# Performance work log

Hardware: AMD Instinct MI355X
Metric: run time of the kernel (lower is better)

## Reference

```python
import jax, jax.numpy as jnp
import numpy as np
from jax import lax

HEADS = 8
HEAD_C = 16  # attention_channels // heads = 128 // 8


def setup_inputs() -> dict:
    key = jax.random.key(0)
    ks = jax.random.split(key, 16)
    N, I, H, W = 8, 128, 36, 36
    R, C, A, O = 128, 128, 128, 128  # recurrent, common, attention, out channels
    s = lambda *sh: 0.05
    inp = {
        'x': jax.random.normal(ks[0], (N, I, H, W), jnp.float32),
        # input 1x1 conv (Accumulate of single Conv, bias init 0)
        'w_in': jax.random.normal(ks[1], (R, I), jnp.float32) * 0.05,
        'b_in': jnp.zeros((R,), jnp.float32),
        # 3x3 conv on cat([x, h]) -> common channels
        'w_conv': jax.random.normal(ks[2], (C, 2 * R, 3, 3), jnp.float32) * 0.05,
        'b_conv': jnp.zeros((C,), jnp.float32),
        # q/k/v 1x1 projections (no bias)
        'wq': jax.random.normal(ks[3], (A, C), jnp.float32) * 0.05,
        'wk': jax.random.normal(ks[4], (A, C), jnp.float32) * 0.05,
        'wv': jax.random.normal(ks[5], (A, C), jnp.float32) * 0.05,
        # gate 1x1 projections on cat([z, a]) (C + A inputs)
        'w_i': jax.random.normal(ks[6], (R, C + A), jnp.float32) * 0.05,
        'b_i': jnp.full((R,), -1.0, jnp.float32),  # init_input
        'w_f': jax.random.normal(ks[7], (R, C + A), jnp.float32) * 0.05,
        'b_f': jnp.full((R,), 1.0, jnp.float32),   # init_forget
        'w_g': jax.random.normal(ks[8], (R, C + A), jnp.float32) * 0.05,
        'b_g': jnp.zeros((R,), jnp.float32),
        'w_o': jax.random.normal(ks[9], (R, C + A), jnp.float32) * 0.05,
        'b_o': jnp.zeros((R,), jnp.float32),
        # output 1x1 conv
        'w_out': jax.random.normal(ks[10], (O, R), jnp.float32) * 0.05,
        'b_out': jnp.zeros((O,), jnp.float32),
    }
    return inp


def _conv1x1(w, x, b=None):
    y = jnp.einsum('oi,nihw->nohw', w, x)
    if b is not None:
        y = y + b[None, :, None, None]
    return y


def reference(x, w_in, b_in, w_conv, b_conv, wq, wk, wv,
              w_i, b_i, w_f, b_f, w_g, b_g, w_o, b_o, w_out, b_out):
    # first timestep: past is empty -> h = c = 0
    xt = jnp.tanh(_conv1x1(w_in, x, b_in))          # [N, R, H, W]
    h0 = jnp.zeros_like(xt)
    c0 = jnp.zeros_like(xt)
    xh = jnp.concatenate([xt, h0], axis=1)          # groups=1 -> plain concat
    z = lax.conv_general_dilated(xh, w_conv, (1, 1), 'SAME') + b_conv[None, :, None, None]
    N, C, H, W = z.shape
    HW = H * W
    q = _conv1x1(wq, z).reshape(N, HEADS, HEAD_C, HW)
    k = _conv1x1(wk, z).reshape(N, HEADS, HEAD_C, HW)
    v = _conv1x1(wv, z).reshape(N, HEADS, HEAD_C, HW)
    # spatial attention over H*W tokens per head
    w_attn = jax.nn.softmax(jnp.einsum('nhcq,nhcd->nhqd', q, k), axis=-1)  # [N,heads,HW,HW]
    a = jnp.einsum('nhcd,nhqd->nhcq', v, w_attn).reshape(N, -1, H, W)      # [N,A,H,W]
    za = jnp.concatenate([z, a], axis=1)
    i = jax.nn.sigmoid(_conv1x1(w_i, za, b_i))
    f = jax.nn.sigmoid(_conv1x1(w_f, za, b_f))
    g = jnp.tanh(_conv1x1(w_g, za, b_g))
    o = jax.nn.sigmoid(_conv1x1(w_o, za, b_o))
    c = f * c0 + i * g
    h = o * jnp.tanh(c)  # dropout p=0 -> identity
    return _conv1x1(w_out, h, b_out)
```

## Files before the change

### kernel.cpp

```cpp
#include <hip/hip_runtime.h>
#include <hip/hip_bf16.h>
#include <math.h>

typedef __hip_bfloat16 bf16;
typedef __attribute__((ext_vector_type(8))) short frag8;
typedef __attribute__((ext_vector_type(4))) float f32x4;
typedef __attribute__((ext_vector_type(16))) float f32x16;
typedef __attribute__((ext_vector_type(2))) unsigned int u32x2;
typedef __attribute__((ext_vector_type(4))) unsigned int u32x4;

#define HW  1296
#define CH  128
#define TT  1327104

__device__ __forceinline__ float b2f(bf16 v) { return __bfloat162float(v); }
__device__ __forceinline__ float bits2f(unsigned short u) {
    return __uint_as_float(((unsigned)u) << 16);
}
__device__ __forceinline__ float frcp(float x) { return __builtin_amdgcn_rcpf(x); }
__device__ __forceinline__ float fsigm(float x) { return frcp(1.0f + __expf(-x)); }
__device__ __forceinline__ float ftanh(float x) {
    float xc = fminf(15.0f, fmaxf(-15.0f, x));
    float e = __expf(2.0f * xc);
    return (e - 1.0f) * frcp(e + 1.0f);
}
__device__ __forceinline__ int packrh(float a, float b) {
    unsigned ua = __float_as_uint(a) + 0x8000u;
    unsigned ub = __float_as_uint(b) + 0x8000u;
    return (int)__builtin_amdgcn_perm(ub, ua, 0x07060302);
}
__device__ __forceinline__ int2 pack4(float a, float b, float c, float d) {
    int2 r; r.x = packrh(a, b); r.y = packrh(c, d); return r;
}
__device__ __forceinline__ unsigned cvtpk(float a, float b) {
    unsigned r;
    asm("v_cvt_pk_bf16_f32 %0, %1, %2" : "=v"(r) : "v"(a), "v"(b));
    return r;
}

__device__ __forceinline__ int detect_f32(const void* w) {
    const short4* p = (const short4*)w;
    short4 v = p[threadIdx.x & 63];
    int bad = 0;
    #pragma unroll
    for (int j = 0; j < 4; ++j) {
        float f = bits2f(((const unsigned short*)&v)[j]);
        if (!(fabsf(f) <= 100.0f)) bad = 1;
    }
    return __any(bad) ? 1 : 0;
}

__global__ __launch_bounds__(256) void k_prep(
    const void* w_in, const void* w_conv, const void* wq, const void* wk, const void* wv,
    const void* w_i, const void* w_g, const void* w_o, const void* w_out,
    const void* b_in, const void* b_conv, const void* b_i, const void* b_g,
    const void* b_o, const void* b_out,
    bf16* __restrict__ Wdst, float* __restrict__ Bdst)
{
    int idx = blockIdx.x * 256 + threadIdx.x;
    const int f = detect_f32(w_in);
    if (idx < 327680) {
        const void* src; int si;
        if (idx < 16384)       { src = w_in; si = idx; }
        else if (idx < 163840) { int j = idx - 16384; int tap = j >> 14, rem = j & 16383;
                                 int o = rem >> 7, r = rem & 127;
                                 src = w_conv; si = o * 2304 + r * 9 + tap; }
        else if (idx < 212992) { int j = idx - 163840; int o = j >> 7, i = j & 127;
                                 int ws_ = o >> 7;
                                 src = ws_ == 0 ? wq : ws_ == 1 ? wk : wv;
                                 si = (o & 127) * 128 + i; }
        else if (idx < 311296) { int j = idx - 212992; int g = j >> 15, rem = j & 32767;
                                 int o = rem >> 8, k = rem & 255;
                                 src = g == 0 ? w_i : g == 1 ? w_g : w_o; si = o * 256 + k; }
        else                   { int j = idx - 311296; int o = j >> 7, i = j & 127;
                                 src = w_out; si = o * 128 + i; }
        float v = f ? ((const float*)src)[si] : b2f(((const bf16*)src)[si]);
        if (idx >= 163840 && idx < 180224) v *= 1.4426950408889634f;
        Wdst[idx] = __float2bfloat16(v);
    } else if (idx < 327680 + 768) {
        int j = idx - 327680; int b = j >> 7, e = j & 127;
        const void* src = b == 0 ? b_in : b == 1 ? b_conv : b == 2 ? b_i
                        : b == 3 ? b_g : b == 4 ? b_o : b_out;
        Bdst[j] = f ? ((const float*)src)[e] : b2f(((const bf16*)src)[e]);
    }
}

__global__ __launch_bounds__(256) void k_inm(const void* __restrict__ x,
                                             const void* __restrict__ wraw,
                                             const bf16* __restrict__ Wm,
                                             const float* __restrict__ bias,
                                             bf16* __restrict__ XT) {
    __shared__ short Xl[32][132];
    const int tid = threadIdx.x, wave = tid >> 6, lane = tid & 63;
    const int quad = lane >> 4, l16 = lane & 15;
    const int n = blockIdx.x;
    const int pbase = blockIdx.y * 32;
    const int obase = blockIdx.z * 32 + (wave & 1) * 16;
    const int pstrip = (wave >> 1) * 16;
    const int f = detect_f32(wraw);

    frag8 WF[4];
    #pragma unroll
    for (int kc = 0; kc < 4; ++kc)
        WF[kc] = *(const frag8*)&Wm[(obase + l16) * CH + kc * 32 + quad * 8];

    #pragma unroll
    for (int rep = 0; rep < 4; ++rep) {
        int u = tid + rep * 256;
        int i = u >> 3;
        int p4 = (u & 7) * 4;
        int p = pbase + p4;
        short4 s = {0, 0, 0, 0};
        if (p < HW) {
            size_t gi = (size_t)n * CH * HW + (size_t)i * HW + p;
            if (f) {
                float4 fv = *(const float4*)((const float*)x + gi);
                int2 pk = pack4(fv.x, fv.y, fv.z, fv.w);
                s = *(short4*)&pk;
            } else {
                s = *(const short4*)((const bf16*)x + gi);
            }
        }
        Xl[p4 + 0][i] = s.x; Xl[p4 + 1][i] = s.y;
        Xl[p4 + 2][i] = s.z; Xl[p4 + 3][i] = s.w;
    }
    __syncthreads();

    const int pl = pstrip + l16;
    f32x4 acc = {0.f, 0.f, 0.f, 0.f};
    #pragma unroll
    for (int kc = 0; kc < 4; ++kc) {
        int k = kc * 32 + quad * 8;
        short4 b0 = *(const short4*)&Xl[pl][k];
        short4 b1 = *(const short4*)&Xl[pl][k + 4];
        frag8 bf = {b0.x, b0.y, b0.z, b0.w, b1.x, b1.y, b1.z, b1.w};
        acc = __builtin_amdgcn_mfma_f32_16x16x32_bf16(WF[kc], bf, acc, 0, 0, 0);
    }

    int p = pbase + pstrip + l16;
    if (p < HW) {
        int og = obase + quad * 4;
        int2 pk = pack4(ftanh(acc[0] + bias[og + 0]), ftanh(acc[1] + bias[og + 1]),
                        ftanh(acc[2] + bias[og + 2]), ftanh(acc[3] + bias[og + 3]));
        *(int2*)((short*)XT + ((size_t)n * HW + p) * CH + og) = pk;
    }
}

__global__ __launch_bounds__(512) void k_cq(
    const bf16* __restrict__ XT, const bf16* __restrict__ Wc,
    const float* __restrict__ bc, const bf16* __restrict__ Wqkv,
    bf16* __restrict__ Zb, bf16* __restrict__ Qb, bf16* __restrict__ Kb,
    bf16* __restrict__ Vb)
{
    __shared__ short Zl[32][136];
    __shared__ float Rd[4][4][4][64];
    const int tid = threadIdx.x, w = tid >> 6, lane = tid & 63;
    const int quad = lane >> 4, l16 = lane & 15;
    const int n = blockIdx.x;
    const int pbase = blockIdx.y * 32;
    const bf16* actn = XT + (size_t)n * HW * CH;

    const int o4 = w & 3, tg = w >> 2;
    const int obase = o4 * 32;
    const int p1 = pbase + l16, p2 = pbase + 16 + l16;
    const bool p1ok = p1 < HW, p2ok = p2 < HW;
    const int h1 = p1 / 36, w1 = p1 - h1 * 36;
    const int h2 = p2 / 36, w2 = p2 - h2 * 36;

    frag8 zf = {0, 0, 0, 0, 0, 0, 0, 0};
    f32x4 acc[2][2];
    #pragma unroll
    for (int of = 0; of < 2; ++of) {
        acc[of][0] = (f32x4){0.f, 0.f, 0.f, 0.f};
        acc[of][1] = (f32x4){0.f, 0.f, 0.f, 0.f};
    }

    const int tap0 = tg ? 5 : 0, tap1 = tg ? 9 : 5;
    for (int tap = tap0; tap < tap1; ++tap) {
        const int dy = tap / 3 - 1, dx = tap - (tap / 3) * 3 - 1;
        const bool ok1 = p1ok && (unsigned)(h1 + dy) < 36u && (unsigned)(w1 + dx) < 36u;
        const bool ok2 = p2ok && (unsigned)(h2 + dy) < 36u && (unsigned)(w2 + dx) < 36u;
        const int sh = dy * 36 + dx;
        const bf16* a1 = actn + (size_t)(p1 + sh) * CH + quad * 8;
        const bf16* a2 = actn + (size_t)(p2 + sh) * CH + quad * 8;
        const bf16* wp0 = Wc + tap * 16384 + (obase + l16) * CH + quad * 8;
        const bf16* wp1 = Wc + tap * 16384 + (obase + 16 + l16) * CH + quad * 8;
        frag8 A1[4], A2[4], W0[4], W1[4];
        #pragma unroll
        for (int kc = 0; kc < 4; ++kc) {
            A1[kc] = ok1 ? *(const frag8*)&a1[kc * 32] : zf;
            A2[kc] = ok2 ? *(const frag8*)&a2[kc * 32] : zf;
            W0[kc] = *(const frag8*)&wp0[kc * 32];
            W1[kc] = *(const frag8*)&wp1[kc * 32];
        }
        #pragma unroll
        for (int kc = 0; kc < 4; ++kc) {
            acc[0][0] = __builtin_amdgcn_mfma_f32_16x16x32_bf16(W0[kc], A1[kc], acc[0][0], 0, 0, 0);
            acc[0][1] = __builtin_amdgcn_mfma_f32_16x16x32_bf16(W0[kc], A2[kc], acc[0][1], 0, 0, 0);
            acc[1][0] = __builtin_amdgcn_mfma_f32_16x16x32_bf16(W1[kc], A1[kc], acc[1][0], 0, 0, 0);
            acc[1][1] = __builtin_amdgcn_mfma_f32_16x16x32_bf16(W1[kc], A2[kc], acc[1][1], 0, 0, 0);
        }
    }

    if (tg == 1) {
        #pragma unroll
        for (int of = 0; of < 2; ++of)
            #pragma unroll
            for (int pt = 0; pt < 2; ++pt)
                #pragma unroll
                for (int r = 0; r < 4; ++r)
                    Rd[o4][of * 2 + pt][r][lane] = acc[of][pt][r];
    }
    __syncthreads();
    if (tg == 0) {
        #pragma unroll
        for (int of = 0; of < 2; ++of) {
            #pragma unroll
            for (int pt = 0; pt < 2; ++pt) {
                #pragma unroll
                for (int r = 0; r < 4; ++r)
                    acc[of][pt][r] += Rd[o4][of * 2 + pt][r][lane];
                int og = obase + of * 16 + quad * 4;
                int pl = pt * 16 + l16;
                int p = pbase + pl;
                int2 pk = pack4(acc[of][pt][0] + bc[og + 0], acc[of][pt][1] + bc[og + 1],
                                acc[of][pt][2] + bc[og + 2], acc[of][pt][3] + bc[og + 3]);
                *(int2*)&Zl[pl][og] = pk;
                if (p < HW)
                    *(int2*)((short*)Zb + ((size_t)n * HW + p) * CH + og) = pk;
            }
        }
    }
    __syncthreads();

    for (int ot = w; ot < 12; ot += 8) {
        const bool vt = (ot >= 8);
        const int ob = ot * 32;
        frag8 B1[4], B2[4], W0a[4], W1a[4];
        #pragma unroll
        for (int kc = 0; kc < 4; ++kc) {
            int ko = kc * 32 + quad * 8;
            B1[kc]  = *(const frag8*)&Zl[l16][ko];
            B2[kc]  = *(const frag8*)&Zl[16 + l16][ko];
            W0a[kc] = *(const frag8*)&Wqkv[(size_t)(ob + l16) * CH + ko];
            W1a[kc] = *(const frag8*)&Wqkv[(size_t)(ob + 16 + l16) * CH + ko];
        }

        f32x4 qacc[2][2];
        #pragma unroll
        for (int of = 0; of < 2; ++of) {
            qacc[of][0] = (f32x4){0.f, 0.f, 0.f, 0.f};
            qacc[of][1] = (f32x4){0.f, 0.f, 0.f, 0.f};
        }
        #pragma unroll
        for (int kc = 0; kc < 4; ++kc) {
            if (vt) {
                qacc[0][0] = __builtin_amdgcn_mfma_f32_16x16x32_bf16(B1[kc], W0a[kc], qacc[0][0], 0, 0, 0);
                qacc[0][1] = __builtin_amdgcn_mfma_f32_16x16x32_bf16(B2[kc], W0a[kc], qacc[0][1], 0, 0, 0);
                qacc[1][0] = __builtin_amdgcn_mfma_f32_16x16x32_bf16(B1[kc], W1a[kc], qacc[1][0], 0, 0, 0);
                qacc[1][1] = __builtin_amdgcn_mfma_f32_16x16x32_bf16(B2[kc], W1a[kc], qacc[1][1], 0, 0, 0);
            } else {
                qacc[0][0] = __builtin_amdgcn_mfma_f32_16x16x32_bf16(W0a[kc], B1[kc], qacc[0][0], 0, 0, 0);
                qacc[0][1] = __builtin_amdgcn_mfma_f32_16x16x32_bf16(W0a[kc], B2[kc], qacc[0][1], 0, 0, 0);
                qacc[1][0] = __builtin_amdgcn_mfma_f32_16x16x32_bf16(W1a[kc], B1[kc], qacc[1][0], 0, 0, 0);
                qacc[1][1] = __builtin_amdgcn_mfma_f32_16x16x32_bf16(W1a[kc], B2[kc], qacc[1][1], 0, 0, 0);
            }
        }

        if (vt) {
            #pragma unroll
            for (int of = 0; of < 2; ++of) {
                int ov = ob + of * 16 - 256 + l16;
                #pragma unroll
                for (int pt = 0; pt < 2; ++pt) {
                    int p4 = pbase + pt * 16 + quad * 4;
                    if (p4 >= HW) continue;
                    int2 pk = pack4(qacc[of][pt][0], qacc[of][pt][1], qacc[of][pt][2], qacc[of][pt][3]);
                    *(int2*)((short*)Vb + ((size_t)n * CH + ov) * HW + p4) = pk;
                }
            }
        } else {
            #pragma unroll
            for (int of = 0; of < 2; ++of) {
                int ogq = ob + of * 16 + quad * 4;
                int which = ogq >> 7, ol = ogq & 127;
                bf16* dst = which == 0 ? Qb : Kb;
                #pragma unroll
                for (int pt = 0; pt < 2; ++pt) {
                    int p = pbase + pt * 16 + l16;
                    if (p >= HW) continue;
                    size_t di = (((size_t)n * 8 + (ol >> 4)) * HW + p) * 16 + (ol & 15);
                    int2 pk = pack4(qacc[of][pt][0], qacc[of][pt][1], qacc[of][pt][2], qacc[of][pt][3]);
                    *(int2*)((short*)dst + di) = pk;
                }
            }
        }
    }
}

__global__ __launch_bounds__(256) void k_cell(
    const bf16* __restrict__ Zb, const bf16* __restrict__ Ab,
    const bf16* __restrict__ Wg, const float* __restrict__ bg,
    const bf16* __restrict__ Wo, const float* __restrict__ bo,
    void* __restrict__ out, const void* __restrict__ wraw)
{
    __shared__ short Hl[16][136];
    const int tid = threadIdx.x, w = tid >> 6, lane = tid & 63;
    const int quad = lane >> 4, l16 = lane & 15;
    const int n = blockIdx.x;
    const int pbase = blockIdx.y * 16;
    const int f32f = detect_f32(wraw);
    const bf16* zn = Zb + (size_t)n * HW * CH;
    const bf16* an = Ab + (size_t)n * HW * CH;

    const int obase = w * 32;
    const int p1 = pbase + l16;

    f32x4 acc[3][2];
    #pragma unroll
    for (int g = 0; g < 3; ++g) {
        acc[g][0] = (f32x4){0.f, 0.f, 0.f, 0.f};
        acc[g][1] = (f32x4){0.f, 0.f, 0.f, 0.f};
    }

    frag8 GB[2];
    frag8 GW[2][6];

    #define LOADG(KC, BUF)                                                           \
    {                                                                                \
        const bf16* src = ((KC) >= 4) ? an : zn;                                     \
        const int ko = ((KC) & 3) * 32 + quad * 8;                                   \
        GB[BUF] = *(const frag8*)&src[(size_t)p1 * CH + ko];                         \
        _Pragma("unroll")                                                            \
        for (int g = 0; g < 3; ++g) {                                                \
            _Pragma("unroll")                                                        \
            for (int of = 0; of < 2; ++of)                                           \
                GW[BUF][g * 2 + of] = *(const frag8*)&Wg[g * 32768 +                 \
                    (obase + of * 16 + l16) * 256 + (KC) * 32 + quad * 8];           \
        }                                                                            \
    }

    LOADG(0, 0);
    #pragma unroll
    for (int kc = 0; kc < 8; ++kc) {
        const int cur = kc & 1;
        if (kc < 7) LOADG(kc + 1, cur ^ 1);
        #pragma unroll
        for (int g = 0; g < 3; ++g) {
            #pragma unroll
            for (int of = 0; of < 2; ++of)
                acc[g][of] = __builtin_amdgcn_mfma_f32_16x16x32_bf16(
                    GW[cur][g * 2 + of], GB[cur], acc[g][of], 0, 0, 0);
        }
    }
    #undef LOADG

    #pragma unroll
    for (int of = 0; of < 2; ++of) {
        int og = obase + of * 16 + quad * 4;
        float hv[4];
        #pragma unroll
        for (int r = 0; r < 4; ++r) {
            int o = og + r;
            float iv = fsigm(acc[0][of][r] + bg[o]);
            float gv = ftanh(acc[1][of][r] + bg[128 + o]);
            float ov = fsigm(acc[2][of][r] + bg[256 + o]);
            hv[r] = ov * ftanh(iv * gv);
        }
        *(int2*)&Hl[l16][og] = pack4(hv[0], hv[1], hv[2], hv[3]);
    }

    frag8 OW[2][4];
    #pragma unroll
    for (int of = 0; of < 2; ++of)
        #pragma unroll
        for (int kc = 0; kc < 4; ++kc)
            OW[of][kc] = *(const frag8*)&Wo[(size_t)(obase + of * 16 + l16) * CH
                                            + kc * 32 + quad * 8];
    __syncthreads();

    f32x4 oc[2];
    oc[0] = (f32x4){0.f, 0.f, 0.f, 0.f};
    oc[1] = (f32x4){0.f, 0.f, 0.f, 0.f};
    #pragma unroll
    for (int kc = 0; kc < 4; ++kc) {
        int k = kc * 32 + quad * 8;
        short4 h0 = *(const short4*)&Hl[l16][k];
        short4 h1 = *(const short4*)&Hl[l16][k + 4];
        frag8 af = {h0.x, h0.y, h0.z, h0.w, h1.x, h1.y, h1.z, h1.w};
        #pragma unroll
        for (int of = 0; of < 2; ++of)
            oc[of] = __builtin_amdgcn_mfma_f32_16x16x32_bf16(af, OW[of][kc], oc[of], 0, 0, 0);
    }
    int p4 = pbase + quad * 4;
    #pragma unroll
    for (int of = 0; of < 2; ++of) {
        int o = obase + of * 16 + l16;
        float bv = bo[o];
        size_t di = ((size_t)n * CH + o) * HW + p4;
        if (f32f) {
            float4 fv = {oc[of][0] + bv, oc[of][1] + bv, oc[of][2] + bv, oc[of][3] + bv};
            *(float4*)&((float*)out)[di] = fv;
        } else {
            int2 pk = pack4(oc[of][0] + bv, oc[of][1] + bv, oc[of][2] + bv, oc[of][3] + bv);
            *(int2*)&((short*)out)[di] = pk;
        }
    }
}

__global__ __launch_bounds__(512) void k_attn(const bf16* __restrict__ Qg,
                                              const bf16* __restrict__ Kg,
                                              const bf16* __restrict__ Vcf,
                                              bf16* __restrict__ A) {
    __shared__ float Lc[4][9][64];

    const int tid = threadIdx.x;
    const int w = tid >> 6, lane = tid & 63;
    const int l32 = lane & 31, hi = lane >> 5;
    const int qw = w & 3, dq = w >> 2;
    const int n = blockIdx.x;
    const int head = blockIdx.z;
    const int qb = blockIdx.y * 128 + qw * 32;
    const int qtok = qb + l32;

    const short* Qh = (const short*)Qg + ((size_t)(n * 8 + head)) * HW * 16;
    const short* Kh = (const short*)Kg + ((size_t)(n * 8 + head)) * HW * 16;
    const short* Vh = (const short*)Vcf + ((size_t)n * CH + head * 16) * HW;

    frag8 qf = {0, 0, 0, 0, 0, 0, 0, 0};
    if (qtok < HW) qf = *(const frag8*)&Qh[(size_t)qtok * 16 + hi * 8];

    const short one = (short)0x3F80;
    const frag8 vones = {one, one, one, one, one, one, one, one};
    const frag8 vzero = {0, 0, 0, 0, 0, 0, 0, 0};
    const frag8 vfill = (l32 == 16) ? vones : vzero;
    const bool vload = l32 < 16;
    const short* Vrow = Vh + (size_t)(vload ? l32 : 0) * HW;

    const f32x16 zero16 = {};
    f32x16 Oacc = {};

    auto KLD = [&](int dd) -> frag8 {
        return *(const frag8*)&Kh[(size_t)(dd + l32) * 16 + hi * 8];
    };
    auto VLD = [&](int dd) -> frag8 {
        return vload ? *(const frag8*)&Vrow[dd + hi * 8] : vfill;
    };

    const int c0 = dq ? 20 : 0;
    frag8 kf  = KLD(c0 * 32);
    frag8 kf2 = KLD(c0 * 32 + 32);
    frag8 va  = VLD(c0 * 32);
    frag8 vb  = VLD(c0 * 32 + 16);
    f32x16 S = __builtin_amdgcn_mfma_f32_32x32x16_bf16(kf, qf, zero16, 0, 0, 0);

    for (int it = 0; it < 20; ++it) {
        const int d0 = (c0 + it) * 32;
        frag8 kn  = KLD(d0 + 64);
        frag8 van = VLD(d0 + 32);
        frag8 vbn = VLD(d0 + 48);
        f32x16 Sn = __builtin_amdgcn_mfma_f32_32x32x16_bf16(kf2, qf, zero16, 0, 0, 0);

        float p[16];
        #pragma unroll
        for (int r = 0; r < 16; ++r) p[r] = __builtin_amdgcn_exp2f(S[r]);

        #pragma unroll
        for (int hh = 0; hh < 2; ++hh) {
            unsigned P0 = cvtpk(p[hh * 8 + 0], p[hh * 8 + 1]);
            unsigned P1 = cvtpk(p[hh * 8 + 2], p[hh * 8 + 3]);
            unsigned P2 = cvtpk(p[hh * 8 + 4], p[hh * 8 + 5]);
            unsigned P3 = cvtpk(p[hh * 8 + 6], p[hh * 8 + 7]);
            u32x2 s02 = __builtin_amdgcn_permlane32_swap(P0, P2, false, false);
            u32x2 s13 = __builtin_amdgcn_permlane32_swap(P1, P3, false, false);
            u32x4 bw = {s02[0], s13[0], s02[1], s13[1]};
            frag8 pf = __builtin_bit_cast(frag8, bw);
            Oacc = __builtin_amdgcn_mfma_f32_32x32x16_bf16(hh ? vb : va, pf, Oacc, 0, 0, 0);
        }
        kf2 = kn; va = van; vb = vbn; S = Sn;
    }

    if (dq) {
        float p[8];
        #pragma unroll
        for (int r = 0; r < 8; ++r) p[r] = __builtin_amdgcn_exp2f(S[r]);
        unsigned P0 = cvtpk(p[0], p[1]);
        unsigned P1 = cvtpk(p[2], p[3]);
        unsigned P2 = cvtpk(p[4], p[5]);
        unsigned P3 = cvtpk(p[6], p[7]);
        u32x2 s02 = __builtin_amdgcn_permlane32_swap(P0, P2, false, false);
        u32x2 s13 = __builtin_amdgcn_permlane32_swap(P1, P3, false, false);
        u32x4 bw = {s02[0], s13[0], s02[1], s13[1]};
        frag8 pf = __builtin_bit_cast(frag8, bw);
        Oacc = __builtin_amdgcn_mfma_f32_32x32x16_bf16(va, pf, Oacc, 0, 0, 0);
        #pragma unroll
        for (int r = 0; r < 8; ++r) Lc[qw][r][lane] = Oacc[r];
        Lc[qw][8][lane] = Oacc[8];
    }
    __syncthreads();
    if (dq == 0) {
        #pragma unroll
        for (int r = 0; r < 8; ++r) Oacc[r] += Lc[qw][r][lane];
        float lsum = Oacc[8] + Lc[qw][8][lane];
        u32x2 lb = __builtin_amdgcn_permlane32_swap(__float_as_uint(lsum),
                                                    __float_as_uint(lsum), false, false);
        float inv = frcp(__uint_as_float(lb[0]));
        if (qtok < HW) {
            short* An = (short*)A + ((size_t)n * HW + qtok) * CH + head * 16;
            int2 pk0 = pack4(Oacc[0] * inv, Oacc[1] * inv, Oacc[2] * inv, Oacc[3] * inv);
            int2 pk1 = pack4(Oacc[4] * inv, Oacc[5] * inv, Oacc[6] * inv, Oacc[7] * inv);
            *(int2*)&An[hi * 4] = pk0;
            *(int2*)&An[8 + hi * 4] = pk1;
        }
    }
}

extern "C" void kernel_launch(void* const* d_in, const int* in_sizes, int n_in,
                              void* d_out, int out_size, void* d_ws, size_t ws_size,
                              hipStream_t stream) {
    char* ws = (char*)d_ws;
    bf16*  Wst  = (bf16*)(ws + 256);
    float* Bst  = (float*)(ws + 655616);
    bf16*  XT   = (bf16*)(ws + 1048576);
    bf16*  Zb   = XT + TT;
    bf16*  Qb   = Zb + TT;
    bf16*  Kb   = Qb + TT;
    bf16*  Vb   = Kb + TT;
    bf16*  Ab   = Vb + TT;

    k_prep<<<1284, 256, 0, stream>>>(d_in[1], d_in[3], d_in[5], d_in[6], d_in[7],
                                     d_in[8], d_in[12], d_in[14], d_in[16],
                                     d_in[2], d_in[4], d_in[9], d_in[13], d_in[15], d_in[17],
                                     Wst, Bst);
    k_inm<<<dim3(8, 41, 4), 256, 0, stream>>>(d_in[0], d_in[1], Wst, Bst, XT);
    k_cq<<<dim3(8, 41), 512, 0, stream>>>(XT, Wst + 16384, Bst + 128, Wst + 163840,
                                          Zb, Qb, Kb, Vb);
    k_attn<<<dim3(8, 11, 8), 512, 0, stream>>>(Qb, Kb, Vb, Ab);
    k_cell<<<dim3(8, 81), 256, 0, stream>>>(Zb, Ab, Wst + 212992, Bst + 256,
                                            Wst + 311296, Bst + 640, d_out, d_in[1]);
}
```

Measured before the change: 185.0 us.

## Split K across more waves in conv and gate kernels with LDS reductions

```diff
diff --git a/kernel.cpp b/kernel.cpp
--- a/kernel.cpp
+++ b/kernel.cpp
@@ -146,14 +146,14 @@
     }
 }
 
-__global__ __launch_bounds__(512) void k_cq(
+__global__ __launch_bounds__(1024) void k_cq(
     const bf16* __restrict__ XT, const bf16* __restrict__ Wc,
     const float* __restrict__ bc, const bf16* __restrict__ Wqkv,
     bf16* __restrict__ Zb, bf16* __restrict__ Qb, bf16* __restrict__ Kb,
     bf16* __restrict__ Vb)
 {
     __shared__ short Zl[32][136];
-    __shared__ float Rd[4][4][4][64];
+    __shared__ float Rd[4][3][4][4][64];
     const int tid = threadIdx.x, w = tid >> 6, lane = tid & 63;
     const int quad = lane >> 4, l16 = lane & 15;
     const int n = blockIdx.x;
@@ -175,7 +175,8 @@
         acc[of][1] = (f32x4){0.f, 0.f, 0.f, 0.f};
     }
 
-    const int tap0 = tg ? 5 : 0, tap1 = tg ? 9 : 5;
+    const int tap0 = tg * 2;
+    const int tap1 = (tg == 3) ? 9 : tap0 + 2;
     for (int tap = tap0; tap < tap1; ++tap) {
         const int dy = tap / 3 - 1, dx = tap - (tap / 3) * 3 - 1;
         const bool ok1 = p1ok && (unsigned)(h1 + dy) < 36u && (unsigned)(w1 + dx) < 36u;
@@ -202,14 +203,14 @@
         }
     }
 
-    if (tg == 1) {
+    if (tg > 0) {
         #pragma unroll
         for (int of = 0; of < 2; ++of)
             #pragma unroll
             for (int pt = 0; pt < 2; ++pt)
                 #pragma unroll
                 for (int r = 0; r < 4; ++r)
-                    Rd[o4][of * 2 + pt][r][lane] = acc[of][pt][r];
+                    Rd[o4][tg - 1][of * 2 + pt][r][lane] = acc[of][pt][r];
     }
     __syncthreads();
     if (tg == 0) {
@@ -218,8 +219,10 @@
             #pragma unroll
             for (int pt = 0; pt < 2; ++pt) {
                 #pragma unroll
-                for (int r = 0; r < 4; ++r)
-                    acc[of][pt][r] += Rd[o4][of * 2 + pt][r][lane];
+                for (int s = 0; s < 3; ++s)
+                    #pragma unroll
+                    for (int r = 0; r < 4; ++r)
+                        acc[of][pt][r] += Rd[o4][s][of * 2 + pt][r][lane];
                 int og = obase + of * 16 + quad * 4;
                 int pl = pt * 16 + l16;
                 int p = pbase + pl;
@@ -233,7 +236,8 @@
     }
     __syncthreads();
 
-    for (int ot = w; ot < 12; ot += 8) {
+    if (w < 12) {
+        const int ot = w;
         const bool vt = (ot >= 8);
         const int ob = ot * 32;
         frag8 B1[4], B2[4], W0a[4], W1a[4];
@@ -298,13 +302,14 @@
     }
 }
 
-__global__ __launch_bounds__(256) void k_cell(
+__global__ __launch_bounds__(512) void k_cell(
     const bf16* __restrict__ Zb, const bf16* __restrict__ Ab,
     const bf16* __restrict__ Wg, const float* __restrict__ bg,
     const bf16* __restrict__ Wo, const float* __restrict__ bo,
     void* __restrict__ out, const void* __restrict__ wraw)
 {
     __shared__ short Hl[16][136];
+    __shared__ float Rd[4][6][4][64];
     const int tid = threadIdx.x, w = tid >> 6, lane = tid & 63;
     const int quad = lane >> 4, l16 = lane & 15;
     const int n = blockIdx.x;
@@ -313,7 +318,8 @@
     const bf16* zn = Zb + (size_t)n * HW * CH;
     const bf16* an = Ab + (size_t)n * HW * CH;
 
-    const int obase = w * 32;
+    const int o4 = w & 3, kg = w >> 2;
+    const int obase = o4 * 32;
     const int p1 = pbase + l16;
 
     f32x4 acc[3][2];
@@ -328,23 +334,24 @@
 
     #define LOADG(KC, BUF)                                                           \
     {                                                                                \
-        const bf16* src = ((KC) >= 4) ? an : zn;                                     \
-        const int ko = ((KC) & 3) * 32 + quad * 8;                                   \
+        const int kcv = (KC);                                                        \
+        const bf16* src = (kcv >= 4) ? an : zn;                                      \
+        const int ko = (kcv & 3) * 32 + quad * 8;                                    \
         GB[BUF] = *(const frag8*)&src[(size_t)p1 * CH + ko];                         \
         _Pragma("unroll")                                                            \
         for (int g = 0; g < 3; ++g) {                                                \
             _Pragma("unroll")                                                        \
             for (int of = 0; of < 2; ++of)                                           \
                 GW[BUF][g * 2 + of] = *(const frag8*)&Wg[g * 32768 +                 \
-                    (obase + of * 16 + l16) * 256 + (KC) * 32 + quad * 8];           \
+                    (obase + of * 16 + l16) * 256 + kcv * 32 + quad * 8];            \
         }                                                                            \
     }
 
-    LOADG(0, 0);
-    #pragma unroll
-    for (int kc = 0; kc < 8; ++kc) {
-        const int cur = kc & 1;
-        if (kc < 7) LOADG(kc + 1, cur ^ 1);
+    LOADG(kg * 4, 0);
+    #pragma unroll
+    for (int i = 0; i < 4; ++i) {
+        const int cur = i & 1;
+        if (i < 3) LOADG(kg * 4 + i + 1, cur ^ 1);
         #pragma unroll
         for (int g = 0; g < 3; ++g) {
             #pragma unroll
@@ -355,55 +362,69 @@
     }
     #undef LOADG
 
-    #pragma unroll
-    for (int of = 0; of < 2; ++of) {
-        int og = obase + of * 16 + quad * 4;
-        float hv[4];
-        #pragma unroll
-        for (int r = 0; r < 4; ++r) {
-            int o = og + r;
-            float iv = fsigm(acc[0][of][r] + bg[o]);
-            float gv = ftanh(acc[1][of][r] + bg[128 + o]);
-            float ov = fsigm(acc[2][of][r] + bg[256 + o]);
-            hv[r] = ov * ftanh(iv * gv);
-        }
-        *(int2*)&Hl[l16][og] = pack4(hv[0], hv[1], hv[2], hv[3]);
-    }
+    if (kg == 1) {
+        #pragma unroll
+        for (int g = 0; g < 3; ++g)
+            #pragma unroll
+            for (int of = 0; of < 2; ++of)
+                #pragma unroll
+                for (int r = 0; r < 4; ++r)
+                    Rd[o4][g * 2 + of][r][lane] = acc[g][of][r];
+    }
+    __syncthreads();
 
     frag8 OW[2][4];
-    #pragma unroll
-    for (int of = 0; of < 2; ++of)
-        #pragma unroll
-        for (int kc = 0; kc < 4; ++kc)
-            OW[of][kc] = *(const frag8*)&Wo[(size_t)(obase + of * 16 + l16) * CH
-                                            + kc * 32 + quad * 8];
+    if (kg == 0) {
+        #pragma unroll
+        for (int of = 0; of < 2; ++of) {
+            int og = obase + of * 16 + quad * 4;
+            float hv[4];
+            #pragma unroll
+            for (int r = 0; r < 4; ++r) {
+                int o = og + r;
+                float iv = fsigm(acc[0][of][r] + Rd[o4][0 * 2 + of][r][lane] + bg[o]);
+                float gv = ftanh(acc[1][of][r] + Rd[o4][1 * 2 + of][r][lane] + bg[128 + o]);
+                float ov = fsigm(acc[2][of][r] + Rd[o4][2 * 2 + of][r][lane] + bg[256 + o]);
+                hv[r] = ov * ftanh(iv * gv);
+            }
+            *(int2*)&Hl[l16][og] = pack4(hv[0], hv[1], hv[2], hv[3]);
+        }
+        #pragma unroll
+        for (int of = 0; of < 2; ++of)
+            #pragma unroll
+            for (int kc = 0; kc < 4; ++kc)
+                OW[of][kc] = *(const frag8*)&Wo[(size_t)(obase + of * 16 + l16) * CH
+                                                + kc * 32 + quad * 8];
+    }
     __syncthreads();
 
-    f32x4 oc[2];
-    oc[0] = (f32x4){0.f, 0.f, 0.f, 0.f};
-    oc[1] = (f32x4){0.f, 0.f, 0.f, 0.f};
-    #pragma unroll
-    for (int kc = 0; kc < 4; ++kc) {
-        int k = kc * 32 + quad * 8;
-        short4 h0 = *(const short4*)&Hl[l16][k];
-        short4 h1 = *(const short4*)&Hl[l16][k + 4];
-        frag8 af = {h0.x, h0.y, h0.z, h0.w, h1.x, h1.y, h1.z, h1.w};
-        #pragma unroll
-        for (int of = 0; of < 2; ++of)
-            oc[of] = __builtin_amdgcn_mfma_f32_16x16x32_bf16(af, OW[of][kc], oc[of], 0, 0, 0);
-    }
-    int p4 = pbase + quad * 4;
-    #pragma unroll
-    for (int of = 0; of < 2; ++of) {
-        int o = obase + of * 16 + l16;
-        float bv = bo[o];
-        size_t di = ((size_t)n * CH + o) * HW + p4;
-        if (f32f) {
-            float4 fv = {oc[of][0] + bv, oc[of][1] + bv, oc[of][2] + bv, oc[of][3] + bv};
-            *(float4*)&((float*)out)[di] = fv;
-        } else {
-            int2 pk = pack4(oc[of][0] + bv, oc[of][1] + bv, oc[of][2] + bv, oc[of][3] + bv);
-            *(int2*)&((short*)out)[di] = pk;
+    if (kg == 0) {
+        f32x4 oc[2];
+        oc[0] = (f32x4){0.f, 0.f, 0.f, 0.f};
+        oc[1] = (f32x4){0.f, 0.f, 0.f, 0.f};
+        #pragma unroll
+        for (int kc = 0; kc < 4; ++kc) {
+            int k = kc * 32 + quad * 8;
+            short4 h0 = *(const short4*)&Hl[l16][k];
+            short4 h1 = *(const short4*)&Hl[l16][k + 4];
+            frag8 af = {h0.x, h0.y, h0.z, h0.w, h1.x, h1.y, h1.z, h1.w};
+            #pragma unroll
+            for (int of = 0; of < 2; ++of)
+                oc[of] = __builtin_amdgcn_mfma_f32_16x16x32_bf16(af, OW[of][kc], oc[of], 0, 0, 0);
+        }
+        int p4 = pbase + quad * 4;
+        #pragma unroll
+        for (int of = 0; of < 2; ++of) {
+            int o = obase + of * 16 + l16;
+            float bv = bo[o];
+            size_t di = ((size_t)n * CH + o) * HW + p4;
+            if (f32f) {
+                float4 fv = {oc[of][0] + bv, oc[of][1] + bv, oc[of][2] + bv, oc[of][3] + bv};
+                *(float4*)&((float*)out)[di] = fv;
+            } else {
+                int2 pk = pack4(oc[of][0] + bv, oc[of][1] + bv, oc[of][2] + bv, oc[of][3] + bv);
+                *(int2*)&((short*)out)[di] = pk;
+            }
         }
     }
 }
@@ -533,9 +554,9 @@
                                      d_in[2], d_in[4], d_in[9], d_in[13], d_in[15], d_in[17],
                                      Wst, Bst);
     k_inm<<<dim3(8, 41, 4), 256, 0, stream>>>(d_in[0], d_in[1], Wst, Bst, XT);
-    k_cq<<<dim3(8, 41), 512, 0, stream>>>(XT, Wst + 16384, Bst + 128, Wst + 163840,
-                                          Zb, Qb, Kb, Vb);
+    k_cq<<<dim3(8, 41), 1024, 0, stream>>>(XT, Wst + 16384, Bst + 128, Wst + 163840,
+                                           Zb, Qb, Kb, Vb);
     k_attn<<<dim3(8, 11, 8), 512, 0, stream>>>(Qb, Kb, Vb, Ab);
-    k_cell<<<dim3(8, 81), 256, 0, stream>>>(Zb, Ab, Wst + 212992, Bst + 256,
+    k_cell<<<dim3(8, 81), 512, 0, stream>>>(Zb, Ab, Wst + 212992, Bst + 256,
                                             Wst + 311296, Bst + 640, d_out, d_in[1]);
 }
```

New measurement: 189.4 us. 1.02x slower.
